# Performance work log

Measured on AMD Instinct MI355X. Metric: run time of the kernel, lower is better.

Reference implementation:

```python
import jax, jax.numpy as jnp
import numpy as np

N_FFT = 1024
N_STAGES = 3
N_SUB = N_FFT >> N_STAGES      # 128-point base IDFT
N_CHUNKS = 1 << N_STAGES       # 8 chunks after partial bit-reversal


def _mod_seq(order):
    mset = [0]
    for o in range(order):
        step = 2 ** o
        mset = [v for x in mset for v in (x, x + step)]
    return mset


def _perm_matrix(N, order):
    m = np.zeros((N, N), dtype=np.float32)
    base = 2 ** order
    k = 0
    for p in _mod_seq(order):
        for j in range(N // base):
            m[j * base + p, k] = 1.0
            k += 1
    return m


PERM = jnp.asarray(_perm_matrix(N_FFT, N_STAGES))
_idft = np.fft.ifft(np.eye(N_SUB))
IDFT_R = jnp.asarray(_idft.real.astype(np.float32))
IDFT_I = jnp.asarray(_idft.imag.astype(np.float32))


def _twiddle(n_fft_stage):
    w = np.exp(2j * np.pi / n_fft_stage) ** np.arange(n_fft_stage // 2)  # inverse sign
    return (jnp.asarray(w.real.astype(np.float32)),
            jnp.asarray(w.imag.astype(np.float32)))


TWIDDLES = []
_stage_size = N_FFT // 2 ** (N_STAGES - 1)
for _ in range(N_STAGES):
    TWIDDLES.append(_twiddle(_stage_size))
    _stage_size *= 2


def _idft_apply(re, im):
    yr = re @ IDFT_R.T - im @ IDFT_I.T
    yi = re @ IDFT_I.T + im @ IDFT_R.T
    return yr, yi


def _ifft_forward(re, im):
    # partial bit-reversal permutation then chunk
    re_p = jnp.split(re @ PERM, N_CHUNKS, axis=-1)
    im_p = jnp.split(im @ PERM, N_CHUNKS, axis=-1)
    ev_r, ev_i, od_r, od_i = [], [], [], []
    for j in range(N_CHUNKS // 2):
        er, ei = _idft_apply(re_p[2 * j], im_p[2 * j])
        o_r, o_i = _idft_apply(re_p[2 * j + 1], im_p[2 * j + 1])
        ev_r.append(er); ev_i.append(ei); od_r.append(o_r); od_i.append(o_i)
    # butterfly twiddle stages
    for tr, ti in TWIDDLES:
        ner, nei, nor, noi = [], [], [], []
        for i in range(len(ev_r)):
            todd_r = tr * od_r[i] - ti * od_i[i]
            todd_i = tr * od_i[i] + ti * od_r[i]
            real = jnp.concatenate([ev_r[i] + todd_r, ev_r[i] - todd_r], axis=-1)
            imag = jnp.concatenate([ev_i[i] + todd_i, ev_i[i] - todd_i], axis=-1)
            if i % 2 == 0:
                ner.append(real); nei.append(imag)
            else:
                nor.append(real); noi.append(imag)
        ev_r, ev_i, od_r, od_i = ner, nei, nor, noi
    scale = 1.0 / (1 << N_STAGES)  # IFFTNormalizer
    return ev_r[0] * scale, ev_i[0] * scale


def setup_inputs() -> dict:
    key = jax.random.key(0)
    k1, k2 = jax.random.split(key)
    re = jax.random.normal(k1, (8, 4096, N_FFT), dtype=jnp.float32)
    im = jax.random.normal(k2, (8, 4096, N_FFT), dtype=jnp.float32)
    return {"re": re, "im": im}


def reference(re, im):
    return _ifft_forward(re, im)
```

## Files before the change

kernel.cpp:

```cpp
#include <hip/hip_runtime.h>

#define NFFT 1024
#define NT   256
__device__ __forceinline__ int swz(int a) { return a + (a >> 5); }

template<int L, int M>
__device__ __forceinline__ void stage(const float* __restrict__ xr,
                                      const float* __restrict__ xi,
                                      float* __restrict__ yr,
                                      float* __restrict__ yi,
                                      int t) {
    const int k  = t & (M - 1);
    const int j  = t / M;
    const int rb = swz(t);

    float c0r = xr[rb];        float c0i = xi[rb];
    float c1r = xr[rb + 264];  float c1i = xi[rb + 264];
    float c2r = xr[rb + 528];  float c2i = xi[rb + 528];
    float c3r = xr[rb + 792];  float c3i = xi[rb + 792];

    float d0r = c0r + c2r, d0i = c0i + c2i;
    float d1r = c0r - c2r, d1i = c0i - c2i;
    float d2r = c1r + c3r, d2i = c1i + c3i;
    float d3r = c3i - c1i, d3i = c1r - c3r;

    float e0r = d0r + d2r, e0i = d0i + d2i;
    float e2r = d0r - d2r, e2i = d0i - d2i;
    float e1r = d1r + d3r, e1i = d1i + d3i;
    float e3r = d1r - d3r, e3i = d1i - d3i;

    float o1r, o1i, o2r, o2i, o3r, o3i;
    if (L == 1) {
        o1r = e1r; o1i = e1i; o2r = e2r; o2i = e2i; o3r = e3r; o3i = e3i;
    } else {
        const float base_ang = 6.28318530717958647692f / (float)(4 * L);
        float ang = base_ang * (float)j;
        float w1i, w1r;
        __sincosf(ang, &w1i, &w1r);
        float w2r = w1r * w1r - w1i * w1i;
        float w2i = 2.0f * w1r * w1i;
        float w3r = w2r * w1r - w2i * w1i;
        float w3i = w2r * w1i + w2i * w1r;
        o1r = w1r * e1r - w1i * e1i;  o1i = w1r * e1i + w1i * e1r;
        o2r = w2r * e2r - w2i * e2i;  o2i = w2r * e2i + w2i * e2r;
        o3r = w3r * e3r - w3i * e3i;  o3i = w3r * e3i + w3i * e3r;
    }

    const int wb = k + 4 * j * M;
    yr[swz(wb)]         = e0r;  yi[swz(wb)]         = e0i;
    yr[swz(wb + M)]     = o1r;  yi[swz(wb + M)]     = o1i;
    yr[swz(wb + 2 * M)] = o2r;  yi[swz(wb + 2 * M)] = o2i;
    yr[swz(wb + 3 * M)] = o3r;  yi[swz(wb + 3 * M)] = o3i;
}

__global__ __launch_bounds__(NT, 8) void ifft1024_kernel(
        const float* __restrict__ re, const float* __restrict__ im,
        float* __restrict__ out, size_t im_out_off) {
    __shared__ float Ar[1056], Ai[1056], Br[1056], Bi[1056];

    const int t = threadIdx.x;
    const size_t base = (size_t)blockIdx.x * NFFT;

    float4 r4 = *(const float4*)(re + base + 4 * t);
    float4 i4 = *(const float4*)(im + base + 4 * t);
    const int p = swz(4 * t);
    Ar[p] = r4.x; Ar[p + 1] = r4.y; Ar[p + 2] = r4.z; Ar[p + 3] = r4.w;
    Ai[p] = i4.x; Ai[p + 1] = i4.y; Ai[p + 2] = i4.z; Ai[p + 3] = i4.w;
    __syncthreads();

    stage<256, 1 >(Ar, Ai, Br, Bi, t); __syncthreads();
    stage<64,  4 >(Br, Bi, Ar, Ai, t); __syncthreads();
    stage<16,  16>(Ar, Ai, Br, Bi, t); __syncthreads();
    stage<4,   64>(Br, Bi, Ar, Ai, t); __syncthreads();
    stage<1,  256>(Ar, Ai, Br, Bi, t); __syncthreads();

    const float s = 1.0f / 1024.0f;
    float4 ro, io;
    ro.x = Br[p] * s; ro.y = Br[p + 1] * s; ro.z = Br[p + 2] * s; ro.w = Br[p + 3] * s;
    io.x = Bi[p] * s; io.y = Bi[p + 1] * s; io.z = Bi[p + 2] * s; io.w = Bi[p + 3] * s;

    *(float4*)(out + base + 4 * t)              = ro;
    *(float4*)(out + im_out_off + base + 4 * t) = io;
}

extern "C" void kernel_launch(void* const* d_in, const int* in_sizes, int n_in,
                              void* d_out, int out_size, void* d_ws, size_t ws_size,
                              hipStream_t stream) {
    const float* re = (const float*)d_in[0];
    const float* im = (const float*)d_in[1];
    float* out = (float*)d_out;
    const int rows = in_sizes[0] / NFFT;
    const size_t im_off = (size_t)in_sizes[0];

    hipLaunchKernelGGL(ifft1024_kernel, dim3(rows), dim3(NT), 0, stream,
                       re, im, out, im_off);
}
```

Baseline: 423.4 us.

## Restructure IFFT as register-resident radix-16 passes with one wavefront per row

Replaces the five shared-memory radix-4 stages with 256 threads by a 64-thread kernel where each thread holds 16 complex points in registers and does two radix-4 stages per pass. Only two shared-memory transposes remain, using an XOR swizzle and float4 writes. This cuts LDS traffic and barriers per row. In exchange it uses more registers per thread, gives fewer threads per row, and global loads and stores are now scalar and strided rather than float4.

```diff
diff --git a/kernel.cpp b/kernel.cpp
--- a/kernel.cpp
+++ b/kernel.cpp
@@ -1,86 +1,161 @@
 #include <hip/hip_runtime.h>
 
 #define NFFT 1024
-#define NT   256
-__device__ __forceinline__ int swz(int a) { return a + (a >> 5); }
+#define TWO_PI 6.28318530717958647692f
 
-template<int L, int M>
-__device__ __forceinline__ void stage(const float* __restrict__ xr,
-                                      const float* __restrict__ xi,
-                                      float* __restrict__ yr,
-                                      float* __restrict__ yi,
-                                      int t) {
-    const int k  = t & (M - 1);
-    const int j  = t / M;
-    const int rb = swz(t);
+__device__ __forceinline__ int SW(int a) {
+    return a ^ ((((a >> 5) ^ (a >> 8)) & 7) << 2);
+}
 
-    float c0r = xr[rb];        float c0i = xi[rb];
-    float c1r = xr[rb + 264];  float c1i = xi[rb + 264];
-    float c2r = xr[rb + 528];  float c2i = xi[rb + 528];
-    float c3r = xr[rb + 792];  float c3i = xi[rb + 792];
+__device__ __forceinline__ void bfly4(float& r0, float& i0, float& r1, float& i1,
+                                      float& r2, float& i2, float& r3, float& i3) {
+    float d0r = r0 + r2, d0i = i0 + i2;
+    float d1r = r0 - r2, d1i = i0 - i2;
+    float d2r = r1 + r3, d2i = i1 + i3;
+    float sr  = r1 - r3, si  = i1 - i3;
+    r0 = d0r + d2r; i0 = d0i + d2i;
+    r2 = d0r - d2r; i2 = d0i - d2i;
+    r1 = d1r - si;  i1 = d1i + sr;
+    r3 = d1r + si;  i3 = d1i - sr;
+}
 
-    float d0r = c0r + c2r, d0i = c0i + c2i;
-    float d1r = c0r - c2r, d1i = c0i - c2i;
-    float d2r = c1r + c3r, d2i = c1i + c3i;
-    float d3r = c3i - c1i, d3i = c1r - c3r;
+__device__ __forceinline__ void twmul(float& x, float& y, float c, float s) {
+    float t = x * c - y * s;
+    y = x * s + y * c;
+    x = t;
+}
 
-    float e0r = d0r + d2r, e0i = d0i + d2i;
-    float e2r = d0r - d2r, e2i = d0i - d2i;
-    float e1r = d1r + d3r, e1i = d1i + d3i;
-    float e3r = d1r - d3r, e3i = d1i - d3i;
+__global__ __launch_bounds__(64, 4) void ifft1024_kernel(
+        const float* __restrict__ re, const float* __restrict__ im,
+        float* __restrict__ out, size_t imoff) {
+    __shared__ __align__(16) float lds[2048];
+    const int u = threadIdx.x;
+    const size_t rowb = (size_t)blockIdx.x * NFFT;
 
-    float o1r, o1i, o2r, o2i, o3r, o3i;
-    if (L == 1) {
-        o1r = e1r; o1i = e1i; o2r = e2r; o2i = e2i; o3r = e3r; o3i = e3i;
-    } else {
-        const float base_ang = 6.28318530717958647692f / (float)(4 * L);
-        float ang = base_ang * (float)j;
-        float w1i, w1r;
-        __sincosf(ang, &w1i, &w1r);
-        float w2r = w1r * w1r - w1i * w1i;
-        float w2i = 2.0f * w1r * w1i;
-        float w3r = w2r * w1r - w2i * w1i;
-        float w3i = w2r * w1i + w2i * w1r;
-        o1r = w1r * e1r - w1i * e1i;  o1i = w1r * e1i + w1i * e1r;
-        o2r = w2r * e2r - w2i * e2i;  o2i = w2r * e2i + w2i * e2r;
-        o3r = w3r * e3r - w3i * e3i;  o3i = w3r * e3i + w3i * e3r;
+    float vr[4][4], vi[4][4];
+
+#pragma unroll
+    for (int b = 0; b < 4; ++b)
+#pragma unroll
+        for (int a = 0; a < 4; ++a) {
+            int idx = u + 64 * a + 256 * b;
+            vr[a][b] = re[rowb + idx];
+            vi[a][b] = im[rowb + idx];
+        }
+
+#pragma unroll
+    for (int a = 0; a < 4; ++a) {
+        bfly4(vr[a][0], vi[a][0], vr[a][1], vi[a][1],
+              vr[a][2], vi[a][2], vr[a][3], vi[a][3]);
+        float ang = (TWO_PI / 1024.f) * (float)(u + 64 * a);
+        float s1, c1; __sincosf(ang, &s1, &c1);
+        float c2 = c1 * c1 - s1 * s1, s2 = 2.f * c1 * s1;
+        float c3 = c2 * c1 - s2 * s1, s3 = c2 * s1 + s2 * c1;
+        twmul(vr[a][1], vi[a][1], c1, s1);
+        twmul(vr[a][2], vi[a][2], c2, s2);
+        twmul(vr[a][3], vi[a][3], c3, s3);
     }
 
-    const int wb = k + 4 * j * M;
-    yr[swz(wb)]         = e0r;  yi[swz(wb)]         = e0i;
-    yr[swz(wb + M)]     = o1r;  yi[swz(wb + M)]     = o1i;
-    yr[swz(wb + 2 * M)] = o2r;  yi[swz(wb + 2 * M)] = o2i;
-    yr[swz(wb + 3 * M)] = o3r;  yi[swz(wb + 3 * M)] = o3i;
-}
+    {
+        float ang = (TWO_PI / 256.f) * (float)u;
+        float s1, c1; __sincosf(ang, &s1, &c1);
+        float c2 = c1 * c1 - s1 * s1, s2 = 2.f * c1 * s1;
+        float c3 = c2 * c1 - s2 * s1, s3 = c2 * s1 + s2 * c1;
+#pragma unroll
+        for (int b = 0; b < 4; ++b) {
+            bfly4(vr[0][b], vi[0][b], vr[1][b], vi[1][b],
+                  vr[2][b], vi[2][b], vr[3][b], vi[3][b]);
+            twmul(vr[1][b], vi[1][b], c1, s1);
+            twmul(vr[2][b], vi[2][b], c2, s2);
+            twmul(vr[3][b], vi[3][b], c3, s3);
+        }
+    }
 
-__global__ __launch_bounds__(NT, 8) void ifft1024_kernel(
-        const float* __restrict__ re, const float* __restrict__ im,
-        float* __restrict__ out, size_t im_out_off) {
-    __shared__ float Ar[1056], Ai[1056], Br[1056], Bi[1056];
+#pragma unroll
+    for (int b = 0; b < 4; ++b) {
+        *(float4*)&lds[SW(16 * u + 4 * b)] =
+            make_float4(vr[0][b], vr[1][b], vr[2][b], vr[3][b]);
+        *(float4*)&lds[SW(16 * u + 4 * b + 1024)] =
+            make_float4(vi[0][b], vi[1][b], vi[2][b], vi[3][b]);
+    }
+    __syncthreads();
+    {
+        int lo = (u >> 2) + 16 * (u & 3);
+#pragma unroll
+        for (int b = 0; b < 4; ++b)
+#pragma unroll
+            for (int a = 0; a < 4; ++a) {
+                int q = lo + 64 * a + 256 * b;
+                vr[a][b] = lds[SW(q)];
+                vi[a][b] = lds[SW(q + 1024)];
+            }
+    }
 
-    const int t = threadIdx.x;
-    const size_t base = (size_t)blockIdx.x * NFFT;
+    const int w = u & 3;
+#pragma unroll
+    for (int a = 0; a < 4; ++a) {
+        bfly4(vr[a][0], vi[a][0], vr[a][1], vi[a][1],
+              vr[a][2], vi[a][2], vr[a][3], vi[a][3]);
+        float ang = (TWO_PI / 64.f) * (float)(w + 4 * a);
+        float s1, c1; __sincosf(ang, &s1, &c1);
+        float c2 = c1 * c1 - s1 * s1, s2 = 2.f * c1 * s1;
+        float c3 = c2 * c1 - s2 * s1, s3 = c2 * s1 + s2 * c1;
+        twmul(vr[a][1], vi[a][1], c1, s1);
+        twmul(vr[a][2], vi[a][2], c2, s2);
+        twmul(vr[a][3], vi[a][3], c3, s3);
+    }
 
-    float4 r4 = *(const float4*)(re + base + 4 * t);
-    float4 i4 = *(const float4*)(im + base + 4 * t);
-    const int p = swz(4 * t);
-    Ar[p] = r4.x; Ar[p + 1] = r4.y; Ar[p + 2] = r4.z; Ar[p + 3] = r4.w;
-    Ai[p] = i4.x; Ai[p + 1] = i4.y; Ai[p + 2] = i4.z; Ai[p + 3] = i4.w;
+    {
+        float ang = (TWO_PI / 16.f) * (float)w;
+        float s1, c1; __sincosf(ang, &s1, &c1);
+        float c2 = c1 * c1 - s1 * s1, s2 = 2.f * c1 * s1;
+        float c3 = c2 * c1 - s2 * s1, s3 = c2 * s1 + s2 * c1;
+#pragma unroll
+        for (int b = 0; b < 4; ++b) {
+            bfly4(vr[0][b], vi[0][b], vr[1][b], vi[1][b],
+                  vr[2][b], vi[2][b], vr[3][b], vi[3][b]);
+            twmul(vr[1][b], vi[1][b], c1, s1);
+            twmul(vr[2][b], vi[2][b], c2, s2);
+            twmul(vr[3][b], vi[3][b], c3, s3);
+        }
+    }
     __syncthreads();
 
-    stage<256, 1 >(Ar, Ai, Br, Bi, t); __syncthreads();
-    stage<64,  4 >(Br, Bi, Ar, Ai, t); __syncthreads();
-    stage<16,  16>(Ar, Ai, Br, Bi, t); __syncthreads();
-    stage<4,   64>(Br, Bi, Ar, Ai, t); __syncthreads();
-    stage<1,  256>(Ar, Ai, Br, Bi, t); __syncthreads();
+#pragma unroll
+    for (int a = 0; a < 4; ++a) {
+        *(float4*)&lds[SW(16 * u + 4 * a)] =
+            make_float4(vr[a][0], vr[a][1], vr[a][2], vr[a][3]);
+        *(float4*)&lds[SW(16 * u + 4 * a + 1024)] =
+            make_float4(vi[a][0], vi[a][1], vi[a][2], vi[a][3]);
+    }
+    __syncthreads();
+    {
+        int lo = (u & 3) + 64 * (u >> 2);
+#pragma unroll
+        for (int c = 0; c < 4; ++c)
+#pragma unroll
+            for (int e = 0; e < 4; ++e) {
+                int q = lo + 4 * c + 16 * e;
+                vr[c][e] = lds[SW(q)];
+                vi[c][e] = lds[SW(q + 1024)];
+            }
+    }
 
-    const float s = 1.0f / 1024.0f;
-    float4 ro, io;
-    ro.x = Br[p] * s; ro.y = Br[p + 1] * s; ro.z = Br[p + 2] * s; ro.w = Br[p + 3] * s;
-    io.x = Bi[p] * s; io.y = Bi[p + 1] * s; io.z = Bi[p + 2] * s; io.w = Bi[p + 3] * s;
+#pragma unroll
+    for (int c = 0; c < 4; ++c)
+        bfly4(vr[c][0], vi[c][0], vr[c][1], vi[c][1],
+              vr[c][2], vi[c][2], vr[c][3], vi[c][3]);
 
-    *(float4*)(out + base + 4 * t)              = ro;
-    *(float4*)(out + im_out_off + base + 4 * t) = io;
+    const float sc = 1.f / 1024.f;
+    const int nbase = 16 * (u & 3) + 4 * ((u >> 2) & 3) + (u >> 4);
+#pragma unroll
+    for (int e = 0; e < 4; ++e)
+#pragma unroll
+        for (int c = 0; c < 4; ++c) {
+            int n = nbase + 64 * c + 256 * e;
+            out[rowb + n]         = vr[c][e] * sc;
+            out[imoff + rowb + n] = vi[c][e] * sc;
+        }
 }
 
 extern "C" void kernel_launch(void* const* d_in, const int* in_sizes, int n_in,
@@ -92,6 +167,6 @@
     const int rows = in_sizes[0] / NFFT;
     const size_t im_off = (size_t)in_sizes[0];
 
-    hipLaunchKernelGGL(ifft1024_kernel, dim3(rows), dim3(NT), 0, stream,
+    hipLaunchKernelGGL(ifft1024_kernel, dim3(rows), dim3(64), 0, stream,
                        re, im, out, im_off);
 }
```

Result: slower. 434.5 us (+2.6%).
